# Performance work log

Hardware: AMD Instinct MI355X
Metric: run time of the kernel (lower is better)

## Reference

```python
import jax, jax.numpy as jnp
import numpy as np

N, E, D, ED, H = 50000, 800000, 128, 16, 1
EPS = 1e-5


def setup_inputs() -> dict:
    key = jax.random.key(0)
    ks = jax.random.split(key, 12)
    return {
        "x": jax.random.normal(ks[0], (N, D), jnp.float32),
        "edge_index": jax.random.randint(ks[1], (2, E), 0, N),
        "edge_attr": jax.random.normal(ks[2], (E, ED), jnp.float32),
        # GATv2Conv params
        "W_l": jax.random.normal(ks[3], (D, H * D), jnp.float32) / np.sqrt(D),
        "b_l": jnp.zeros((H * D,), jnp.float32),
        "W_r": jax.random.normal(ks[4], (D, H * D), jnp.float32) / np.sqrt(D),
        "b_r": jnp.zeros((H * D,), jnp.float32),
        "W_e": jax.random.normal(ks[5], (ED, H * D), jnp.float32) / np.sqrt(ED),
        "att": jax.random.normal(ks[6], (H, D), jnp.float32) * 0.1,
        "bias_gat": jnp.zeros((D,), jnp.float32),
        # block params
        "weight1": jax.random.normal(ks[7], (2,), jnp.float32),
        "bn1_gamma": jnp.ones((D,), jnp.float32),
        "bn1_beta": jnp.zeros((D,), jnp.float32),
        "conv_w": jax.random.normal(ks[8], (D, D, 3), jnp.float32) / np.sqrt(3 * D),
        "conv_b": jnp.zeros((D,), jnp.float32),
        "weight2": jax.random.normal(ks[9], (2,), jnp.float32),
        "bn2_gamma": jnp.ones((D,), jnp.float32),
        "bn2_beta": jnp.zeros((D,), jnp.float32),
    }


def _batch_norm(z, gamma, beta):
    # NodeLevelBatchNorm in training mode: stats over all nodes of the batch graph
    mu = z.mean(axis=0)
    var = z.var(axis=0)
    return (z - mu) * jax.lax.rsqrt(var + EPS) * gamma + beta


def _gatv2(x, edge_index, edge_attr, W_l, b_l, W_r, b_r, W_e, att, bias_gat):
    n = x.shape[0]
    # add self loops with edge_attr fill_value=0
    loop = jnp.arange(n)
    src = jnp.concatenate([edge_index[0], loop])  # message sources j
    dst = jnp.concatenate([edge_index[1], loop])  # message targets i
    x_l = (x @ W_l + b_l).reshape(n, H, D)
    x_r = (x @ W_r + b_r).reshape(n, H, D)
    e = (edge_attr @ W_e).reshape(-1, H, D)
    e = jnp.concatenate([e, jnp.zeros((n, H, D), e.dtype)], axis=0)  # zeros: lin_edge(0)=0
    # [E+N, H, D] edge messages
    m = jax.nn.leaky_relu(x_l[src] + x_r[dst] + e, negative_slope=0.2)
    logits = jnp.einsum('ehc,hc->eh', m, att)  # [E+N, H]
    # softmax grouped by target node (every node has a self loop -> no empty segments)
    lmax = jax.ops.segment_max(logits, dst, num_segments=n)
    p = jnp.exp(logits - lmax[dst])
    denom = jax.ops.segment_sum(p, dst, num_segments=n)
    alpha = p / denom[dst]
    out = jax.ops.segment_sum(alpha[:, :, None] * x_l[src], dst, num_segments=n)  # [N,H,D]
    return out.mean(axis=1) + bias_gat  # concat=False -> head mean


def reference(x, edge_index, edge_attr, W_l, b_l, W_r, b_r, W_e, att, bias_gat,
              weight1, bn1_gamma, bn1_beta, conv_w, conv_b, weight2,
              bn2_gamma, bn2_beta):
    attn_feat = _gatv2(x, edge_index, edge_attr, W_l, b_l, W_r, b_r, W_e, att, bias_gat)
    w1 = jax.nn.softmax(weight1)
    z = w1[0] * x + w1[1] * attn_feat
    z = _batch_norm(z, bn1_gamma, bn1_beta)
    # Conv1d over the node dimension: [1, C, N] -> [1, C, N]
    z1 = jax.lax.conv_general_dilated(
        z.T[None], conv_w, window_strides=(1,), padding=[(1, 1)],
        dimension_numbers=('NCH', 'OIH', 'NCH'))
    z1 = z1[0].T + conv_b  # [N, C]
    z1 = jax.nn.leaky_relu(z1, negative_slope=0.01)  # dropout inactive in eval
    w2 = jax.nn.softmax(weight2)
    z = w2[0] * z + w2[1] * z1
    z = _batch_norm(z, bn2_gamma, bn2_beta)
    return z
```

## Files before the change

### kernel.cpp

```cpp
#include <hip/hip_runtime.h>
#include <hip/hip_bf16.h>
#include <math.h>

#define DD 128
#define EPSBN 1e-5f

__device__ __forceinline__ float4 f4_add(float4 a, float4 b) {
    return make_float4(a.x + b.x, a.y + b.y, a.z + b.z, a.w + b.w);
}
__device__ __forceinline__ float4 f4_fma(float a, float4 b, float4 c) {
    c.x = fmaf(a, b.x, c.x); c.y = fmaf(a, b.y, c.y);
    c.z = fmaf(a, b.z, c.z); c.w = fmaf(a, b.w, c.w);
    return c;
}
__device__ __forceinline__ float leakyf(float v, float s) { return v > 0.f ? v : s * v; }

__device__ __forceinline__ unsigned short f2bf(float f) {
    unsigned u = __float_as_uint(f);
    return (unsigned short)((u + 0x7fffu + ((u >> 16) & 1u)) >> 16);
}
__device__ __forceinline__ float2 bf2f2(unsigned u) {
    float2 r;
    r.x = __uint_as_float(u << 16);
    r.y = __uint_as_float(u & 0xFFFF0000u);
    return r;
}

__device__ __forceinline__ void eproj2(const float4* __restrict__ ea4,
                                       const float* __restrict__ wex, const float* __restrict__ wey,
                                       float& ex, float& ey) {
    float4 a0 = ea4[0], a1 = ea4[1], a2 = ea4[2], a3 = ea4[3];
    float ea[16] = {a0.x, a0.y, a0.z, a0.w, a1.x, a1.y, a1.z, a1.w,
                    a2.x, a2.y, a2.z, a2.w, a3.x, a3.y, a3.z, a3.w};
    float x = 0.f, y = 0.f;
    #pragma unroll
    for (int k = 0; k < 16; ++k) {
        x = fmaf(ea[k], wex[k], x);
        y = fmaf(ea[k], wey[k], y);
    }
    ex = x; ey = y;
}

__global__ __launch_bounds__(256) void k_prep(const float* __restrict__ conv_w, float* __restrict__ wT,
                                              int* __restrict__ counts, float* __restrict__ stats,
                                              int n, int nstats) {
    int idx = blockIdx.x * 256 + threadIdx.x;
    if (idx < 3 * 128 * 128) {
        int k = idx >> 14;
        int r = idx & 16383;
        int ci = r >> 7, co = r & 127;
        wT[idx] = conv_w[(size_t)co * 384 + ci * 3 + k];
    }
    int z = idx - 3 * 128 * 128;
    if (z >= 0) {
        if (z < n) counts[z] = 0;
        else if (z - n < nstats) stats[z - n] = 0.f;
    }
}

__global__ __launch_bounds__(256) void k_gemm_xlxr(
    const float* __restrict__ x, const float* __restrict__ Wl, const float* __restrict__ bl,
    const float* __restrict__ Wr, const float* __restrict__ br,
    float* __restrict__ XR, unsigned short* __restrict__ XLh, int n)
{
    __shared__ float As[64 * 33];
    __shared__ float Bs[32 * 256];
    int tid = threadIdx.x;
    int r0 = blockIdx.x * 64;
    int tx = tid & 31, ty = tid >> 5;

    float4 accL[8], accR[8];
    #pragma unroll
    for (int j = 0; j < 8; ++j) {
        accL[j] = make_float4(0.f, 0.f, 0.f, 0.f);
        accR[j] = make_float4(0.f, 0.f, 0.f, 0.f);
    }

    for (int k0 = 0; k0 < 128; k0 += 32) {
        for (int idx = tid; idx < 64 * 32; idx += 256) {
            int lrow = idx >> 5, kk = idx & 31;
            int g = r0 + lrow;
            As[lrow * 33 + kk] = (g < n) ? x[(size_t)g * DD + k0 + kk] : 0.f;
        }
        for (int idx = tid; idx < 2048; idx += 256) {
            int kk = idx >> 6, co4 = idx & 63;
            float4 v;
            if (co4 < 32) v = ((const float4*)Wl)[(size_t)(k0 + kk) * 32 + co4];
            else          v = ((const float4*)Wr)[(size_t)(k0 + kk) * 32 + (co4 - 32)];
            ((float4*)Bs)[kk * 64 + co4] = v;
        }
        __syncthreads();

        #pragma unroll 4
        for (int kk = 0; kk < 32; ++kk) {
            float a[8];
            #pragma unroll
            for (int j = 0; j < 8; ++j) a[j] = As[(ty * 8 + j) * 33 + kk];
            float4 bL = ((float4*)Bs)[kk * 64 + tx];
            float4 bR = ((float4*)Bs)[kk * 64 + 32 + tx];
            #pragma unroll
            for (int j = 0; j < 8; ++j) {
                accL[j] = f4_fma(a[j], bL, accL[j]);
                accR[j] = f4_fma(a[j], bR, accR[j]);
            }
        }
        __syncthreads();
    }

    float4 blv = ((const float4*)bl)[tx];
    float4 brv = ((const float4*)br)[tx];
    #pragma unroll
    for (int j = 0; j < 8; ++j) {
        int row = r0 + ty * 8 + j;
        if (row < n) {
            float4 L4 = f4_add(accL[j], blv);
            ((float4*)(XR + (size_t)row * DD))[tx] = f4_add(accR[j], brv);
            uint2 hp;
            hp.x = (unsigned)f2bf(L4.x) | ((unsigned)f2bf(L4.y) << 16);
            hp.y = (unsigned)f2bf(L4.z) | ((unsigned)f2bf(L4.w) << 16);
            ((uint2*)(XLh + (size_t)row * DD))[tx] = hp;
        }
    }
}

__global__ __launch_bounds__(256) void k_hist(const int* __restrict__ dst, int* __restrict__ counts, int e) {
    int idx = blockIdx.x * 256 + threadIdx.x;
    if (idx < e) atomicAdd(&counts[dst[idx]], 1);
}

__global__ __launch_bounds__(256) void k_scan1(const int* __restrict__ counts,
                                               int* __restrict__ offsets, int* __restrict__ bsum, int n) {
    __shared__ int tmp[256];
    int t = threadIdx.x;
    int i = blockIdx.x * 256 + t;
    int v = (i < n) ? counts[i] : 0;
    tmp[t] = v;
    __syncthreads();
    for (int off = 1; off < 256; off <<= 1) {
        int u = (t >= off) ? tmp[t - off] : 0;
        __syncthreads();
        tmp[t] += u;
        __syncthreads();
    }
    if (i < n) offsets[i] = tmp[t] - v;
    if (t == 255) bsum[blockIdx.x] = tmp[255];
}

__global__ __launch_bounds__(1024) void k_scan2(int* __restrict__ bsum, int nchunks) {
    __shared__ int tmp[1024];
    int t = threadIdx.x;
    int v = (t < nchunks) ? bsum[t] : 0;
    tmp[t] = v;
    __syncthreads();
    for (int off = 1; off < 1024; off <<= 1) {
        int u = (t >= off) ? tmp[t - off] : 0;
        __syncthreads();
        tmp[t] += u;
        __syncthreads();
    }
    if (t < nchunks) bsum[t] = tmp[t] - v;
    if (t == 0) bsum[nchunks] = tmp[nchunks - 1];
}

__global__ __launch_bounds__(256) void k_scan3(int* __restrict__ offsets, int* __restrict__ cursor,
                                               const int* __restrict__ bsum, int n, int nchunks) {
    int i = blockIdx.x * 256 + threadIdx.x;
    if (i < n) {
        int o = offsets[i] + bsum[i >> 8];
        offsets[i] = o;
        cursor[i] = o;
    }
    if (i == n) offsets[n] = bsum[nchunks];
}

__global__ __launch_bounds__(256) void k_scatter(const int* __restrict__ src, const int* __restrict__ dst,
                                                 int* __restrict__ cursor, int2* __restrict__ epair, int e) {
    int idx = blockIdx.x * 256 + threadIdx.x;
    if (idx >= e) return;
    int d = dst[idx];
    int pos = atomicAdd(&cursor[d], 1);
    epair[pos] = make_int2(idx, src[idx]);
}

__global__ __launch_bounds__(256) void k_gat(
    const unsigned short* __restrict__ XLh, const float* __restrict__ XR,
    const float* __restrict__ x,
    const int2* __restrict__ epair, const int* __restrict__ offsets,
    const float* __restrict__ edge_attr, const float* __restrict__ We,
    const float* __restrict__ att, const float* __restrict__ bias_gat,
    const float* __restrict__ weight1, float* __restrict__ Z, int n, int nwaves)
{
    int wid  = blockIdx.x * 4 + (threadIdx.x >> 6);
    int lane = threadIdx.x & 63;
    int c = lane * 2;

    float wex[16], wey[16];
    #pragma unroll
    for (int k = 0; k < 16; ++k) {
        float2 w = *(const float2*)(We + k * DD + c);
        wex[k] = w.x; wey[k] = w.y;
    }
    float2 att2 = *(const float2*)(att + c);
    float2 bg   = *(const float2*)(bias_gat + c);
    float w0 = weight1[0], w1v = weight1[1];
    float mw = fmaxf(w0, w1v);
    float e0w = __expf(w0 - mw), e1w = __expf(w1v - mw);
    float winv = 1.f / (e0w + e1w);
    float w1x = e0w * winv, w1a = e1w * winv;

    for (int i = wid; i < n; i += nwaves) {
        float2 xr2 = *(const float2*)(XR + (size_t)i * DD + c);
        float2 xli = bf2f2(((const unsigned*)XLh)[(size_t)i * 64 + lane]);

        float sl = leakyf(xli.x + xr2.x, 0.2f) * att2.x + leakyf(xli.y + xr2.y, 0.2f) * att2.y;
        #pragma unroll
        for (int off = 32; off > 0; off >>= 1) sl += __shfl_xor(sl, off, 64);
        float gs = __expf(sl);
        float S = gs, ax = gs * xli.x, ay = gs * xli.y;

        int p = offsets[i], offe = offsets[i + 1];

        for (; p + 2 <= offe; p += 2) {
            int2 ej0 = epair[p], ej1 = epair[p + 1];
            unsigned u0 = ((const unsigned*)XLh)[(size_t)ej0.y * 64 + lane];
            unsigned u1 = ((const unsigned*)XLh)[(size_t)ej1.y * 64 + lane];
            float ex0, ey0, ex1, ey1;
            eproj2((const float4*)edge_attr + (size_t)ej0.x * 4, wex, wey, ex0, ey0);
            eproj2((const float4*)edge_attr + (size_t)ej1.x * 4, wex, wey, ex1, ey1);
            float2 x0 = bf2f2(u0), x1 = bf2f2(u1);
            float l0 = leakyf(x0.x + xr2.x + ex0, 0.2f) * att2.x +
                       leakyf(x0.y + xr2.y + ey0, 0.2f) * att2.y;
            float l1 = leakyf(x1.x + xr2.x + ex1, 0.2f) * att2.x +
                       leakyf(x1.y + xr2.y + ey1, 0.2f) * att2.y;
            #pragma unroll
            for (int off = 32; off > 0; off >>= 1) {
                l0 += __shfl_xor(l0, off, 64);
                l1 += __shfl_xor(l1, off, 64);
            }
            float g0 = __expf(l0), g1 = __expf(l1);
            S  += g0 + g1;
            ax += g0 * x0.x + g1 * x1.x;
            ay += g0 * x0.y + g1 * x1.y;
        }
        if (p < offe) {
            int2 ej = epair[p];
            unsigned u = ((const unsigned*)XLh)[(size_t)ej.y * 64 + lane];
            float ex, ey;
            eproj2((const float4*)edge_attr + (size_t)ej.x * 4, wex, wey, ex, ey);
            float2 x0 = bf2f2(u);
            float l = leakyf(x0.x + xr2.x + ex, 0.2f) * att2.x +
                      leakyf(x0.y + xr2.y + ey, 0.2f) * att2.y;
            #pragma unroll
            for (int off = 32; off > 0; off >>= 1) l += __shfl_xor(l, off, 64);
            float g = __expf(l);
            S += g; ax += g * x0.x; ay += g * x0.y;
        }

        float rl = 1.f / S;
        float axv = fmaf(ax, rl, bg.x), ayv = fmaf(ay, rl, bg.y);
        float2 xv = *(const float2*)(x + (size_t)i * DD + c);
        float2 zv;
        zv.x = w1x * xv.x + w1a * axv;
        zv.y = w1x * xv.y + w1a * ayv;
        *(float2*)(Z + (size_t)i * DD + c) = zv;
    }
}

__global__ __launch_bounds__(256) void k_bn_stats(const float* __restrict__ Zin,
                                                  float* __restrict__ sums, float* __restrict__ sumsq, int n) {
    __shared__ float4 Ls[8][32];
    __shared__ float4 Lq[8][32];
    int tid = threadIdx.x;
    int cg = tid & 31, ry = tid >> 5;
    float4 s = make_float4(0.f, 0.f, 0.f, 0.f), q = s;
    for (int r = blockIdx.x * 8 + ry; r < n; r += gridDim.x * 8) {
        float4 v = ((const float4*)(Zin + (size_t)r * DD))[cg];
        s = f4_add(s, v);
        q.x = fmaf(v.x, v.x, q.x); q.y = fmaf(v.y, v.y, q.y);
        q.z = fmaf(v.z, v.z, q.z); q.w = fmaf(v.w, v.w, q.w);
    }
    Ls[ry][cg] = s; Lq[ry][cg] = q;
    __syncthreads();
    if (tid < 32) {
        float4 ts = Ls[0][tid], tq = Lq[0][tid];
        #pragma unroll
        for (int j = 1; j < 8; ++j) { ts = f4_add(ts, Ls[j][tid]); tq = f4_add(tq, Lq[j][tid]); }
        atomicAdd(&sums[tid * 4 + 0], ts.x); atomicAdd(&sums[tid * 4 + 1], ts.y);
        atomicAdd(&sums[tid * 4 + 2], ts.z); atomicAdd(&sums[tid * 4 + 3], ts.w);
        atomicAdd(&sumsq[tid * 4 + 0], tq.x); atomicAdd(&sumsq[tid * 4 + 1], tq.y);
        atomicAdd(&sumsq[tid * 4 + 2], tq.z); atomicAdd(&sumsq[tid * 4 + 3], tq.w);
    }
}

__global__ __launch_bounds__(128) void k_bn_finish(const float* __restrict__ sums, const float* __restrict__ sumsq,
                                                   const float* __restrict__ gamma, const float* __restrict__ beta,
                                                   float* __restrict__ scale, float* __restrict__ shift, int n) {
    int t = threadIdx.x;
    if (t >= 128) return;
    float fn = (float)n;
    float mu = sums[t] / fn;
    float var = sumsq[t] / fn - mu * mu;
    float rstd = rsqrtf(var + EPSBN);
    float sc = gamma[t] * rstd;
    scale[t] = sc;
    shift[t] = fmaf(-mu, sc, beta[t]);
}

__global__ __launch_bounds__(256) void k_conv(
    const float* __restrict__ Z, const float* __restrict__ scale1, const float* __restrict__ shift1,
    const float* __restrict__ wT, const float* __restrict__ conv_b,
    const float* __restrict__ weight2, float* __restrict__ Z2, int n)
{
    __shared__ float As[66 * 33];
    __shared__ float Bs[3 * 32 * 128];
    int tid = threadIdx.x;
    int r0 = blockIdx.x * 64;
    int tx = tid & 31, ty = tid >> 5;
    int rbase = ty * 8;

    float4 acc[8];
    #pragma unroll
    for (int j = 0; j < 8; ++j) acc[j] = make_float4(0.f, 0.f, 0.f, 0.f);

    for (int ci0 = 0; ci0 < 128; ci0 += 32) {
        for (int idx = tid; idx < 66 * 32; idx += 256) {
            int lrow = idx >> 5, ci = idx & 31;
            int g = r0 - 1 + lrow;
            int cc = ci0 + ci;
            float v = 0.f;
            if (g >= 0 && g < n)
                v = fmaf(Z[(size_t)g * DD + cc], scale1[cc], shift1[cc]);
            As[lrow * 33 + ci] = v;
        }
        for (int idx = tid; idx < 3072; idx += 256) {
            int k = idx >> 10;
            int r = idx & 1023;
            int ci = r >> 5, co4 = r & 31;
            ((float4*)Bs)[idx] = ((const float4*)wT)[(size_t)k * 4096 + (ci0 + ci) * 32 + co4];
        }
        __syncthreads();

        #pragma unroll 2
        for (int ci = 0; ci < 32; ++ci) {
            float a[10];
            #pragma unroll
            for (int j = 0; j < 10; ++j) a[j] = As[(rbase + j) * 33 + ci];
            float4 b0 = ((float4*)Bs)[(0 * 32 + ci) * 32 + tx];
            float4 b1 = ((float4*)Bs)[(1 * 32 + ci) * 32 + tx];
            float4 b2 = ((float4*)Bs)[(2 * 32 + ci) * 32 + tx];
            #pragma unroll
            for (int j = 0; j < 8; ++j) {
                acc[j] = f4_fma(a[j],     b0, acc[j]);
                acc[j] = f4_fma(a[j + 1], b1, acc[j]);
                acc[j] = f4_fma(a[j + 2], b2, acc[j]);
            }
        }
        __syncthreads();
    }

    float w0 = weight2[0], w1v = weight2[1];
    float mw = fmaxf(w0, w1v);
    float e0 = __expf(w0 - mw), e1 = __expf(w1v - mw);
    float winv = 1.f / (e0 + e1);
    float w2x = e0 * winv, w2a = e1 * winv;

    float4 cb = ((const float4*)conv_b)[tx];
    float4 sc1 = ((const float4*)scale1)[tx];
    float4 sh1 = ((const float4*)shift1)[tx];
    #pragma unroll
    for (int j = 0; j < 8; ++j) {
        int row = r0 + rbase + j;
        if (row >= n) break;
        float4 z1 = f4_add(acc[j], cb);
        z1.x = leakyf(z1.x, 0.01f); z1.y = leakyf(z1.y, 0.01f);
        z1.z = leakyf(z1.z, 0.01f); z1.w = leakyf(z1.w, 0.01f);
        float4 zv = ((const float4*)(Z + (size_t)row * DD))[tx];
        float4 zbn;
        zbn.x = fmaf(zv.x, sc1.x, sh1.x); zbn.y = fmaf(zv.y, sc1.y, sh1.y);
        zbn.z = fmaf(zv.z, sc1.z, sh1.z); zbn.w = fmaf(zv.w, sc1.w, sh1.w);
        float4 o;
        o.x = w2x * zbn.x + w2a * z1.x; o.y = w2x * zbn.y + w2a * z1.y;
        o.z = w2x * zbn.z + w2a * z1.z; o.w = w2x * zbn.w + w2a * z1.w;
        ((float4*)(Z2 + (size_t)row * DD))[tx] = o;
    }
}

__global__ __launch_bounds__(256) void k_final(const float* __restrict__ Z2,
                                               const float* __restrict__ scale2, const float* __restrict__ shift2,
                                               float* __restrict__ out, int total4) {
    int idx = blockIdx.x * 256 + threadIdx.x;
    if (idx >= total4) return;
    int c4 = idx & 31;
    float4 v = ((const float4*)Z2)[idx];
    float4 sc = ((const float4*)scale2)[c4];
    float4 sh = ((const float4*)shift2)[c4];
    float4 r;
    r.x = fmaf(v.x, sc.x, sh.x); r.y = fmaf(v.y, sc.y, sh.y);
    r.z = fmaf(v.z, sc.z, sh.z); r.w = fmaf(v.w, sc.w, sh.w);
    ((float4*)out)[idx] = r;
}

extern "C" void kernel_launch(void* const* d_in, const int* in_sizes, int n_in,
                              void* d_out, int out_size, void* d_ws, size_t ws_size,
                              hipStream_t stream)
{
    const float* x          = (const float*)d_in[0];
    const int*   edge_index = (const int*)d_in[1];
    const float* edge_attr  = (const float*)d_in[2];
    const float* W_l        = (const float*)d_in[3];
    const float* b_l        = (const float*)d_in[4];
    const float* W_r        = (const float*)d_in[5];
    const float* b_r        = (const float*)d_in[6];
    const float* W_e        = (const float*)d_in[7];
    const float* att        = (const float*)d_in[8];
    const float* bias_gat   = (const float*)d_in[9];
    const float* weight1    = (const float*)d_in[10];
    const float* bn1_gamma  = (const float*)d_in[11];
    const float* bn1_beta   = (const float*)d_in[12];
    const float* conv_w     = (const float*)d_in[13];
    const float* conv_b     = (const float*)d_in[14];
    const float* weight2    = (const float*)d_in[15];
    const float* bn2_gamma  = (const float*)d_in[16];
    const float* bn2_beta   = (const float*)d_in[17];

    int n = in_sizes[0] / DD;
    int e = in_sizes[1] / 2;
    int nchunks = (n + 255) / 256;

    float* XR = (float*)d_ws;
    float* Z  = XR + (size_t)n * DD;
    float* wT = Z + (size_t)n * DD;
    float* stats = wT + 49152;
    float* sums1 = stats,       *sumsq1 = stats + 128;
    float* sums2 = stats + 256, *sumsq2 = stats + 384;
    float* scale1 = stats + 512, *shift1 = stats + 640;
    float* scale2 = stats + 768, *shift2 = stats + 896;
    int* counts  = (int*)(stats + 1024);
    int* offsets = counts + n;
    int* cursor  = offsets + n + 2;
    int* bsum    = cursor + n;
    int2* epair  = (int2*)(bsum + ((nchunks + 2) & ~1));
    unsigned short* XLh = (unsigned short*)(epair + e);
    float* Z2 = XR;

    const int* src = edge_index;
    const int* dst = edge_index + e;

    const int nwaves = 8192;

    k_prep<<<(3 * 128 * 128 + n + 512 + 255) / 256, 256, 0, stream>>>(conv_w, wT, counts, stats, n, 512);
    k_gemm_xlxr<<<(n + 63) / 64, 256, 0, stream>>>(x, W_l, b_l, W_r, b_r, XR, XLh, n);
    k_hist<<<(e + 255) / 256, 256, 0, stream>>>(dst, counts, e);
    k_scan1<<<nchunks, 256, 0, stream>>>(counts, offsets, bsum, n);
    k_scan2<<<1, 1024, 0, stream>>>(bsum, nchunks);
    k_scan3<<<(n + 256) / 256, 256, 0, stream>>>(offsets, cursor, bsum, n, nchunks);
    k_scatter<<<(e + 255) / 256, 256, 0, stream>>>(src, dst, cursor, epair, e);
    k_gat<<<nwaves / 4, 256, 0, stream>>>(XLh, XR, x, epair, offsets,
                                          edge_attr, W_e, att, bias_gat, weight1, Z, n, nwaves);
    k_bn_stats<<<256, 256, 0, stream>>>(Z, sums1, sumsq1, n);
    k_bn_finish<<<1, 128, 0, stream>>>(sums1, sumsq1, bn1_gamma, bn1_beta, scale1, shift1, n);
    k_conv<<<(n + 63) / 64, 256, 0, stream>>>(Z, scale1, shift1, wT, conv_b, weight2, Z2, n);
    k_bn_stats<<<256, 256, 0, stream>>>(Z2, sums2, sumsq2, n);
    k_bn_finish<<<1, 128, 0, stream>>>(sums2, sumsq2, bn2_gamma, bn2_beta, scale2, shift2, n);
    k_final<<<(n * 32 + 255) / 256, 256, 0, stream>>>(Z2, scale2, shift2, (float*)d_out, n * 32);
}
```

Baseline: 650.5 us.

## Software-pipeline GAT edge loop with scalarized indices and packed float2 math

```diff
diff --git a/kernel.cpp b/kernel.cpp
--- a/kernel.cpp
+++ b/kernel.cpp
@@ -4,6 +4,8 @@
 
 #define DD 128
 #define EPSBN 1e-5f
+
+typedef float f2 __attribute__((ext_vector_type(2)));
 
 __device__ __forceinline__ float4 f4_add(float4 a, float4 b) {
     return make_float4(a.x + b.x, a.y + b.y, a.z + b.z, a.w + b.w);
@@ -19,26 +21,15 @@
     unsigned u = __float_as_uint(f);
     return (unsigned short)((u + 0x7fffu + ((u >> 16) & 1u)) >> 16);
 }
-__device__ __forceinline__ float2 bf2f2(unsigned u) {
-    float2 r;
+__device__ __forceinline__ f2 bfu2f2(unsigned u) {
+    f2 r;
     r.x = __uint_as_float(u << 16);
     r.y = __uint_as_float(u & 0xFFFF0000u);
     return r;
 }
-
-__device__ __forceinline__ void eproj2(const float4* __restrict__ ea4,
-                                       const float* __restrict__ wex, const float* __restrict__ wey,
-                                       float& ex, float& ey) {
-    float4 a0 = ea4[0], a1 = ea4[1], a2 = ea4[2], a3 = ea4[3];
-    float ea[16] = {a0.x, a0.y, a0.z, a0.w, a1.x, a1.y, a1.z, a1.w,
-                    a2.x, a2.y, a2.z, a2.w, a3.x, a3.y, a3.z, a3.w};
-    float x = 0.f, y = 0.f;
-    #pragma unroll
-    for (int k = 0; k < 16; ++k) {
-        x = fmaf(ea[k], wex[k], x);
-        y = fmaf(ea[k], wey[k], y);
-    }
-    ex = x; ey = y;
+__device__ __forceinline__ f2 leaky2(f2 v, float s) {
+    f2 z = (f2)0.f;
+    return __builtin_elementwise_max(v, z) + s * __builtin_elementwise_min(v, z);
 }
 
 __global__ __launch_bounds__(256) void k_prep(const float* __restrict__ conv_w, float* __restrict__ wT,
@@ -182,6 +173,45 @@
     epair[pos] = make_int2(idx, src[idx]);
 }
 
+#define GAT_LOAD(q_, U0_, U1_, A0_, A1_)                                        \
+    {                                                                           \
+        int2 g0_ = epair[q_], g1_ = epair[(q_) + 1];                            \
+        int e0_ = __builtin_amdgcn_readfirstlane(g0_.x);                        \
+        int s0_ = __builtin_amdgcn_readfirstlane(g0_.y);                        \
+        int e1_ = __builtin_amdgcn_readfirstlane(g1_.x);                        \
+        int s1_ = __builtin_amdgcn_readfirstlane(g1_.y);                        \
+        U0_ = XLu[(size_t)s0_ * 64 + lane];                                     \
+        U1_ = XLu[(size_t)s1_ * 64 + lane];                                     \
+        const float* q0_ = edge_attr + (size_t)e0_ * 16;                        \
+        const float* q1_ = edge_attr + (size_t)e1_ * 16;                        \
+        _Pragma("unroll")                                                       \
+        for (int k_ = 0; k_ < 16; ++k_) { A0_[k_] = q0_[k_]; A1_[k_] = q1_[k_]; } \
+    }
+
+#define GAT_COMPUTE(U0_, U1_, A0_, A1_)                                         \
+    {                                                                           \
+        f2 x0_ = bfu2f2(U0_), x1_ = bfu2f2(U1_);                                \
+        f2 ev0_ = (f2)0.f, ev1_ = (f2)0.f;                                      \
+        _Pragma("unroll")                                                       \
+        for (int k_ = 0; k_ < 16; ++k_) {                                       \
+            ev0_ = __builtin_elementwise_fma((f2)A0_[k_], w2[k_], ev0_);        \
+            ev1_ = __builtin_elementwise_fma((f2)A1_[k_], w2[k_], ev1_);        \
+        }                                                                       \
+        f2 m0_ = leaky2(x0_ + xr2 + ev0_, 0.2f);                                \
+        f2 m1_ = leaky2(x1_ + xr2 + ev1_, 0.2f);                                \
+        float l0_ = m0_.x * att2.x + m0_.y * att2.y;                            \
+        float l1_ = m1_.x * att2.x + m1_.y * att2.y;                            \
+        _Pragma("unroll")                                                       \
+        for (int off_ = 32; off_ > 0; off_ >>= 1) {                             \
+            l0_ += __shfl_xor(l0_, off_, 64);                                   \
+            l1_ += __shfl_xor(l1_, off_, 64);                                   \
+        }                                                                       \
+        float g0_ = __expf(l0_), g1_ = __expf(l1_);                             \
+        S += g0_ + g1_;                                                         \
+        axy = __builtin_elementwise_fma((f2)g0_, x0_, axy);                     \
+        axy = __builtin_elementwise_fma((f2)g1_, x1_, axy);                     \
+    }
+
 __global__ __launch_bounds__(256) void k_gat(
     const unsigned short* __restrict__ XLh, const float* __restrict__ XR,
     const float* __restrict__ x,
@@ -193,15 +223,13 @@
     int wid  = blockIdx.x * 4 + (threadIdx.x >> 6);
     int lane = threadIdx.x & 63;
     int c = lane * 2;
-
-    float wex[16], wey[16];
+    const unsigned* __restrict__ XLu = (const unsigned*)XLh;
+
+    f2 w2[16];
     #pragma unroll
-    for (int k = 0; k < 16; ++k) {
-        float2 w = *(const float2*)(We + k * DD + c);
-        wex[k] = w.x; wey[k] = w.y;
-    }
-    float2 att2 = *(const float2*)(att + c);
-    float2 bg   = *(const float2*)(bias_gat + c);
+    for (int k = 0; k < 16; ++k) w2[k] = *(const f2*)(We + k * DD + c);
+    f2 att2 = *(const f2*)(att + c);
+    f2 bg   = *(const f2*)(bias_gat + c);
     float w0 = weight1[0], w1v = weight1[1];
     float mw = fmaxf(w0, w1v);
     float e0w = __expf(w0 - mw), e1w = __expf(w1v - mw);
@@ -209,60 +237,61 @@
     float w1x = e0w * winv, w1a = e1w * winv;
 
     for (int i = wid; i < n; i += nwaves) {
-        float2 xr2 = *(const float2*)(XR + (size_t)i * DD + c);
-        float2 xli = bf2f2(((const unsigned*)XLh)[(size_t)i * 64 + lane]);
-
-        float sl = leakyf(xli.x + xr2.x, 0.2f) * att2.x + leakyf(xli.y + xr2.y, 0.2f) * att2.y;
+        f2 xr2 = *(const f2*)(XR + (size_t)i * DD + c);
+        f2 xli = bfu2f2(XLu[(size_t)i * 64 + lane]);
+
+        f2 ms = leaky2(xli + xr2, 0.2f);
+        float sl = ms.x * att2.x + ms.y * att2.y;
         #pragma unroll
         for (int off = 32; off > 0; off >>= 1) sl += __shfl_xor(sl, off, 64);
         float gs = __expf(sl);
-        float S = gs, ax = gs * xli.x, ay = gs * xli.y;
-
-        int p = offsets[i], offe = offsets[i + 1];
-
-        for (; p + 2 <= offe; p += 2) {
-            int2 ej0 = epair[p], ej1 = epair[p + 1];
-            unsigned u0 = ((const unsigned*)XLh)[(size_t)ej0.y * 64 + lane];
-            unsigned u1 = ((const unsigned*)XLh)[(size_t)ej1.y * 64 + lane];
-            float ex0, ey0, ex1, ey1;
-            eproj2((const float4*)edge_attr + (size_t)ej0.x * 4, wex, wey, ex0, ey0);
-            eproj2((const float4*)edge_attr + (size_t)ej1.x * 4, wex, wey, ex1, ey1);
-            float2 x0 = bf2f2(u0), x1 = bf2f2(u1);
-            float l0 = leakyf(x0.x + xr2.x + ex0, 0.2f) * att2.x +
-                       leakyf(x0.y + xr2.y + ey0, 0.2f) * att2.y;
-            float l1 = leakyf(x1.x + xr2.x + ex1, 0.2f) * att2.x +
-                       leakyf(x1.y + xr2.y + ey1, 0.2f) * att2.y;
-            #pragma unroll
-            for (int off = 32; off > 0; off >>= 1) {
-                l0 += __shfl_xor(l0, off, 64);
-                l1 += __shfl_xor(l1, off, 64);
+        float S = gs;
+        f2 axy = gs * xli;
+
+        int p  = __builtin_amdgcn_readfirstlane(offsets[i]);
+        int pe = __builtin_amdgcn_readfirstlane(offsets[i + 1]);
+        int cnt = pe - p;
+        int np = cnt >> 1;
+
+        unsigned uA0, uA1, uB0, uB1;
+        float aA0[16], aA1[16], aB0[16], aB1[16];
+
+        if (np > 0) {
+            GAT_LOAD(p, uA0, uA1, aA0, aA1);
+            int t = 0;
+            for (;;) {
+                if (t + 1 < np) GAT_LOAD(p + 2 * (t + 1), uB0, uB1, aB0, aB1);
+                GAT_COMPUTE(uA0, uA1, aA0, aA1);
+                if (++t >= np) break;
+                if (t + 1 < np) GAT_LOAD(p + 2 * (t + 1), uA0, uA1, aA0, aA1);
+                GAT_COMPUTE(uB0, uB1, aB0, aB1);
+                if (++t >= np) break;
             }
-            float g0 = __expf(l0), g1 = __expf(l1);
-            S  += g0 + g1;
-            ax += g0 * x0.x + g1 * x1.x;
-            ay += g0 * x0.y + g1 * x1.y;
-        }
-        if (p < offe) {
-            int2 ej = epair[p];
-            unsigned u = ((const unsigned*)XLh)[(size_t)ej.y * 64 + lane];
-            float ex, ey;
-            eproj2((const float4*)edge_attr + (size_t)ej.x * 4, wex, wey, ex, ey);
-            float2 x0 = bf2f2(u);
-            float l = leakyf(x0.x + xr2.x + ex, 0.2f) * att2.x +
-                      leakyf(x0.y + xr2.y + ey, 0.2f) * att2.y;
+        }
+        if (cnt & 1) {
+            int2 ej = epair[pe - 1];
+            int eid = __builtin_amdgcn_readfirstlane(ej.x);
+            int srn = __builtin_amdgcn_readfirstlane(ej.y);
+            unsigned u = XLu[(size_t)srn * 64 + lane];
+            const float* pa = edge_attr + (size_t)eid * 16;
+            f2 ev = (f2)0.f;
+            #pragma unroll
+            for (int k = 0; k < 16; ++k) ev = __builtin_elementwise_fma((f2)pa[k], w2[k], ev);
+            f2 x0 = bfu2f2(u);
+            f2 m = leaky2(x0 + xr2 + ev, 0.2f);
+            float l = m.x * att2.x + m.y * att2.y;
             #pragma unroll
             for (int off = 32; off > 0; off >>= 1) l += __shfl_xor(l, off, 64);
             float g = __expf(l);
-            S += g; ax += g * x0.x; ay += g * x0.y;
+            S += g;
+            axy = __builtin_elementwise_fma((f2)g, x0, axy);
         }
 
         float rl = 1.f / S;
-        float axv = fmaf(ax, rl, bg.x), ayv = fmaf(ay, rl, bg.y);
-        float2 xv = *(const float2*)(x + (size_t)i * DD + c);
-        float2 zv;
-        zv.x = w1x * xv.x + w1a * axv;
-        zv.y = w1x * xv.y + w1a * ayv;
-        *(float2*)(Z + (size_t)i * DD + c) = zv;
+        f2 av = axy * rl + bg;
+        f2 xv = *(const f2*)(x + (size_t)i * DD + c);
+        f2 zv = w1x * xv + w1a * av;
+        *(f2*)(Z + (size_t)i * DD + c) = zv;
     }
 }
 
```

Result: faster. 612.9 us (-5.8%).
